# Performance work log

Measured on AMD Instinct MI355X. Metric: run time of the kernel, lower is better.

## Reference

```python
import jax, jax.numpy as jnp
import numpy as np
import math

V, D, H, L, MLP = 32000, 1024, 16, 4, 4
B, T = 2, 1024
HD = D // H
ALIBI_BIAS_MAX = 8.0
EPS = 1e-5


def _ln(x, g, b):
    m = jnp.mean(x, -1, keepdims=True)
    v = jnp.mean((x - m) ** 2, -1, keepdims=True)
    return (x - m) * jax.lax.rsqrt(v + EPS) * g + b


def setup_inputs() -> dict:
    key = jax.random.key(0)
    ks = jax.random.split(key, 12)
    s = 0.02
    inp = {
        "input_ids": jax.random.randint(ks[0], (B, T), 0, V),
        "wte": jax.random.normal(ks[1], (V, D), jnp.float32) * s,
        "ln1_g": jnp.ones((L, D), jnp.float32),
        "ln1_b": jnp.zeros((L, D), jnp.float32),
        "attn_w": jax.random.normal(ks[2], (L, 3 * D, D), jnp.float32) * s,
        "attn_b": jnp.zeros((L, 3 * D), jnp.float32),
        "proj_w": jax.random.normal(ks[3], (L, D, D), jnp.float32) * s,
        "proj_b": jnp.zeros((L, D), jnp.float32),
        "ln2_g": jnp.ones((L, D), jnp.float32),
        "ln2_b": jnp.zeros((L, D), jnp.float32),
        "fc_w": jax.random.normal(ks[4], (L, MLP * D, D), jnp.float32) * s,
        "fc_b": jnp.zeros((L, MLP * D), jnp.float32),
        "fc2_w": jax.random.normal(ks[5], (L, D, MLP * D), jnp.float32) * s,
        "fc2_b": jnp.zeros((L, D), jnp.float32),
        "lnf_g": jnp.ones((D,), jnp.float32),
        "lnf_b": jnp.zeros((D,), jnp.float32),
        "lm_head_w": jax.random.normal(ks[6], (V, D), jnp.float32) * s,
    }
    return inp


def reference(input_ids, wte, ln1_g, ln1_b, attn_w, attn_b, proj_w, proj_b,
              ln2_g, ln2_b, fc_w, fc_b, fc2_w, fc2_b, lnf_g, lnf_b, lm_head_w):
    b, t = input_ids.shape
    x = wte[input_ids]  # [B,T,D]

    # causal + ALiBi bias, [H,T,T]
    pos = jnp.arange(t)
    rel = -jnp.abs(pos[None, :] - pos[:, None]).astype(jnp.float32)  # -|i-j|
    m = jnp.arange(1, H + 1, dtype=jnp.float32) * (ALIBI_BIAS_MAX / H)
    alibi = rel[None, :, :] * (2.0 ** (-m))[:, None, None]
    causal = jnp.where(pos[None, :] > pos[:, None], -jnp.inf, 0.0)
    bias = alibi + causal[None]
    scale = 1.0 / math.sqrt(HD)

    def block(x, p):
        l1g, l1b, aw, ab, pw, pb, l2g, l2b, fw, fb, f2w, f2b = p
        h = _ln(x, l1g, l1b)
        qkv = h @ aw.T + ab  # [B,T,3D]
        q, k, v = jnp.split(qkv, 3, axis=-1)
        q = q.reshape(b, t, H, HD).transpose(0, 2, 1, 3)
        k = k.reshape(b, t, H, HD).transpose(0, 2, 1, 3)
        v = v.reshape(b, t, H, HD).transpose(0, 2, 1, 3)
        att = jnp.einsum('bhid,bhjd->bhij', q, k) * scale + bias[None]
        att = jax.nn.softmax(att, axis=-1)
        y = jnp.einsum('bhij,bhjd->bhid', att, v)
        y = y.transpose(0, 2, 1, 3).reshape(b, t, D)
        x = x + (y @ pw.T + pb)
        h2 = _ln(x, l2g, l2b)
        x = x + (jax.nn.gelu(h2 @ fw.T + fb, approximate=False) @ f2w.T + f2b)
        return x, None

    x, _ = jax.lax.scan(
        block, x,
        (ln1_g, ln1_b, attn_w, attn_b, proj_w, proj_b,
         ln2_g, ln2_b, fc_w, fc_b, fc2_w, fc2_b))
    x = _ln(x, lnf_g, lnf_b)
    logits = x @ lm_head_w.T  # [B,T,V]
    return logits
```

## Files before the change

kernel.cpp:

```cpp
#include <hip/hip_runtime.h>
#include <hip/hip_bf16.h>
#include <math.h>

typedef __hip_bfloat16 bf16;
typedef __attribute__((ext_vector_type(4))) float f32x4;
typedef __attribute__((ext_vector_type(8))) short short8;

constexpr int Bc = 2, Tc = 1024, Dc = 1024, Hc = 16, Lc = 4, MLPc = 4096, Vc = 32000, HDc = 64;

__device__ __forceinline__ unsigned short f2bu(float f) {
    __hip_bfloat16 h = __float2bfloat16(f);
    unsigned short u;
    __builtin_memcpy(&u, &h, 2);
    return u;
}

__device__ __forceinline__ void gl2lds16(const bf16* g, bf16* l) {
    __builtin_amdgcn_global_load_lds(
        (const __attribute__((address_space(1))) void*)g,
        (__attribute__((address_space(3))) void*)l, 16, 0, 0);
}

enum { EPI_BIAS_BF16 = 0, EPI_GELU = 1, EPI_RESADD = 2, EPI_F32 = 3 };

template <int EPI>
__device__ __forceinline__ void epi_store(float v, int row, int col, void* Cv,
                                          int ldc, const float* bias) {
    if constexpr (EPI == EPI_BIAS_BF16) {
        v += bias[col];
        ((bf16*)Cv)[(size_t)row * ldc + col] = __float2bfloat16(v);
    } else if constexpr (EPI == EPI_GELU) {
        v += bias[col];
        v = 0.5f * v * (1.0f + erff(v * 0.70710678118f));
        ((bf16*)Cv)[(size_t)row * ldc + col] = __float2bfloat16(v);
    } else if constexpr (EPI == EPI_RESADD) {
        float* C = (float*)Cv;
        size_t idx = (size_t)row * ldc + col;
        C[idx] += v + bias[col];
    } else if constexpr (EPI == EPI_F32) {
        ((float*)Cv)[(size_t)row * ldc + col] = v;
    }
}

template <int BM, int BN, int BK, int EPI, bool SWZG>
__global__ __launch_bounds__(256) void gemm_fast(
    const bf16* __restrict__ A, int lda,
    const bf16* __restrict__ Bm, int ldb,
    void* __restrict__ Cv, int ldc,
    const float* __restrict__ bias, int K)
{
    static_assert(BK == 64, "staging geometry assumes BK=64");
    __shared__ alignas(16) bf16 As[BM][BK];
    __shared__ alignas(16) bf16 Bs[BN][BK];

    const int tid = threadIdx.x;
    const int lane = tid & 63;
    const int w = tid >> 6;
    const int wm = w >> 1, wn = w & 1;
    constexpr int WM = BM / 2, WN = BN / 2;
    constexpr int FM = WM / 16, FN = WN / 16;
    constexpr int RPI = 512 / BK;
    constexpr int AI = BM / (4 * RPI);
    constexpr int BI = BN / (4 * RPI);

    int im, in;
    if constexpr (SWZG) {
        int nwg = gridDim.x * gridDim.y;
        int orig = blockIdx.y * gridDim.x + blockIdx.x;
        int q = nwg >> 3, rr = nwg & 7, xcd = orig & 7, lid = orig >> 3;
        int wg = (xcd < rr ? xcd * (q + 1) : rr * (q + 1) + (xcd - rr) * q) + lid;
        im = wg % gridDim.x;
        in = wg / gridDim.x;
    } else {
        im = blockIdx.y;
        in = blockIdx.x;
    }

    const bf16* Ab = A + (size_t)im * BM * lda;
    const bf16* Bb = Bm + (size_t)in * BN * ldb;

    const int sr = lane >> 3;
    const int scs = (((lane & 7) ^ sr) * 8);
    const int lr = lane & 15, lq = lane >> 4;

    f32x4 acc[FM][FN];
#pragma unroll
    for (int i = 0; i < FM; i++)
#pragma unroll
        for (int j = 0; j < FN; j++) acc[i][j] = (f32x4){0.f, 0.f, 0.f, 0.f};

    for (int k0 = 0; k0 < K; k0 += BK) {
#pragma unroll
        for (int i = 0; i < AI; i++) {
            int row = (w * AI + i) * RPI;
            gl2lds16(Ab + (size_t)(row + sr) * lda + k0 + scs, &As[row][0]);
        }
#pragma unroll
        for (int i = 0; i < BI; i++) {
            int row = (w * BI + i) * RPI;
            gl2lds16(Bb + (size_t)(row + sr) * ldb + k0 + scs, &Bs[row][0]);
        }
        __syncthreads();

#pragma unroll
        for (int kk = 0; kk < BK / 32; kk++) {
            short8 af[FM], bfr[FN];
#pragma unroll
            for (int i = 0; i < FM; i++) {
                int r = wm * WM + i * 16 + lr;
                int cb = (kk * 64 + lq * 16) ^ ((r & 7) << 4);
                af[i] = *reinterpret_cast<const short8*>((const char*)As + (size_t)r * (BK * 2) + cb);
            }
#pragma unroll
            for (int j = 0; j < FN; j++) {
                int r = wn * WN + j * 16 + lr;
                int cb = (kk * 64 + lq * 16) ^ ((r & 7) << 4);
                bfr[j] = *reinterpret_cast<const short8*>((const char*)Bs + (size_t)r * (BK * 2) + cb);
            }
#pragma unroll
            for (int i = 0; i < FM; i++)
#pragma unroll
                for (int j = 0; j < FN; j++)
                    acc[i][j] = __builtin_amdgcn_mfma_f32_16x16x32_bf16(af[i], bfr[j], acc[i][j], 0, 0, 0);
        }
        __syncthreads();
    }

#pragma unroll
    for (int i = 0; i < FM; i++)
#pragma unroll
        for (int j = 0; j < FN; j++)
#pragma unroll
            for (int r = 0; r < 4; r++) {
                int row = im * BM + wm * WM + i * 16 + lq * 4 + r;
                int col = in * BN + wn * WN + j * 16 + lr;
                epi_store<EPI>(acc[i][j][r], row, col, Cv, ldc, bias);
            }
}

__global__ __launch_bounds__(256) void flash_attn(
    const bf16* __restrict__ q, const bf16* __restrict__ kbuf,
    const bf16* __restrict__ vt, bf16* __restrict__ y)
{
    __shared__ alignas(16) bf16 Ks[128 * 64];
    __shared__ alignas(16) bf16 Vs[64 * 128];
    __shared__ alignas(16) bf16 Ps[4 * 16 * 136];

    const int tid = threadIdx.x;
    const int lane = tid & 63;
    const int w = tid >> 6;
    const int lr = lane & 15, lq = lane >> 4;
    const int qi = (int)gridDim.x - 1 - (int)blockIdx.x;
    const int z = blockIdx.y;
    const int b = z >> 4, h = z & 15;
    const float slope = exp2f(-0.5f * (float)(h + 1));

    const bf16* qz = q + (size_t)z * (Tc * HDc);
    const bf16* kz = kbuf + (size_t)z * (Tc * HDc);
    const bf16* vz = vt + (size_t)z * (HDc * Tc);

    const int rowbase = qi * 64 + w * 16;

    short8 qf[2];
#pragma unroll
    for (int kk = 0; kk < 2; kk++)
        qf[kk] = *reinterpret_cast<const short8*>(
            qz + (size_t)(rowbase + lr) * HDc + kk * 32 + lq * 8);

    float m_old[4], l_sum[4];
#pragma unroll
    for (int r = 0; r < 4; r++) { m_old[r] = -3.0e38f; l_sum[r] = 0.f; }
    f32x4 o[4];
#pragma unroll
    for (int dj = 0; dj < 4; dj++) o[dj] = (f32x4){0.f, 0.f, 0.f, 0.f};

    bf16* Pw = Ps + w * 16 * 136;

    const int nkv = (qi * 64 + 63) / 128 + 1;
    for (int kv = 0; kv < nkv; kv++) {
#pragma unroll
        for (int i = 0; i < 4; i++) {
            int rbase = w * 32 + i * 8;
            int row = rbase + (lane >> 3);
            int slot = lane & 7;
            gl2lds16(kz + (size_t)(kv * 128 + row) * HDc + ((slot ^ (row & 7)) * 8),
                     &Ks[rbase * 64]);
        }
#pragma unroll
        for (int i = 0; i < 4; i++) {
            int rbase = w * 16 + i * 4;
            int row = rbase + lq;
            gl2lds16(vz + (size_t)row * Tc + kv * 128 + ((lr ^ (row & 7)) * 8),
                     &Vs[rbase * 128]);
        }
        __syncthreads();

        f32x4 s[8];
#pragma unroll
        for (int j = 0; j < 8; j++) s[j] = (f32x4){0.f, 0.f, 0.f, 0.f};
#pragma unroll
        for (int kk = 0; kk < 2; kk++) {
#pragma unroll
            for (int j = 0; j < 8; j++) {
                int row = j * 16 + lr;
                int cb = ((kk * 4 + lq) ^ (row & 7)) << 4;
                short8 bfr = *reinterpret_cast<const short8*>(
                    (const char*)Ks + row * 128 + cb);
                s[j] = __builtin_amdgcn_mfma_f32_16x16x32_bf16(qf[kk], bfr, s[j], 0, 0, 0);
            }
        }

        float mt[4];
#pragma unroll
        for (int r = 0; r < 4; r++) mt[r] = -3.0e38f;
#pragma unroll
        for (int j = 0; j < 8; j++) {
            int col = kv * 128 + j * 16 + lr;
#pragma unroll
            for (int r = 0; r < 4; r++) {
                int rowg = rowbase + lq * 4 + r;
                float v = s[j][r] * 0.125f - (float)(rowg - col) * slope;
                v = (col > rowg) ? -3.0e38f : v;
                s[j][r] = v;
                mt[r] = fmaxf(mt[r], v);
            }
        }
#pragma unroll
        for (int r = 0; r < 4; r++)
#pragma unroll
            for (int off = 1; off < 16; off <<= 1)
                mt[r] = fmaxf(mt[r], __shfl_xor(mt[r], off));

        float f[4], rs[4];
#pragma unroll
        for (int r = 0; r < 4; r++) {
            float mn = fmaxf(m_old[r], mt[r]);
            f[r] = __expf(m_old[r] - mn);
            m_old[r] = mn;
            rs[r] = 0.f;
        }
#pragma unroll
        for (int j = 0; j < 8; j++)
#pragma unroll
            for (int r = 0; r < 4; r++) {
                float p = __expf(s[j][r] - m_old[r]);
                s[j][r] = p;
                rs[r] += p;
            }
#pragma unroll
        for (int r = 0; r < 4; r++) {
#pragma unroll
            for (int off = 1; off < 16; off <<= 1)
                rs[r] += __shfl_xor(rs[r], off);
            l_sum[r] = l_sum[r] * f[r] + rs[r];
        }

#pragma unroll
        for (int j = 0; j < 8; j++)
#pragma unroll
            for (int r = 0; r < 4; r++)
                Pw[(lq * 4 + r) * 136 + j * 16 + lr] = __float2bfloat16(s[j][r]);

#pragma unroll
        for (int dj = 0; dj < 4; dj++)
#pragma unroll
            for (int r = 0; r < 4; r++) o[dj][r] *= f[r];

        __syncthreads();

#pragma unroll
        for (int kk = 0; kk < 4; kk++) {
            short8 pa = *reinterpret_cast<const short8*>(
                (const char*)Pw + lr * 272 + kk * 64 + lq * 16);
#pragma unroll
            for (int dj = 0; dj < 4; dj++) {
                int row = dj * 16 + lr;
                int cb = ((kk * 4 + lq) ^ (row & 7)) << 4;
                short8 vb = *reinterpret_cast<const short8*>(
                    (const char*)Vs + row * 256 + cb);
                o[dj] = __builtin_amdgcn_mfma_f32_16x16x32_bf16(pa, vb, o[dj], 0, 0, 0);
            }
        }
        __syncthreads();
    }

#pragma unroll
    for (int dj = 0; dj < 4; dj++)
#pragma unroll
        for (int r = 0; r < 4; r++) {
            int rowg = rowbase + lq * 4 + r;
            float outv = o[dj][r] / l_sum[r];
            y[((size_t)b * Tc + rowg) * Dc + h * HDc + dj * 16 + lr] =
                __float2bfloat16(outv);
        }
}

__global__ __launch_bounds__(256) void f2b8(const float* __restrict__ in,
                                            bf16* __restrict__ out, long n) {
    long i = ((long)blockIdx.x * 256 + threadIdx.x) * 8;
    if (i >= n) return;
    float4 a = *reinterpret_cast<const float4*>(in + i);
    float4 b = *reinterpret_cast<const float4*>(in + i + 4);
    unsigned long long p0 = (unsigned long long)f2bu(a.x) |
                            ((unsigned long long)f2bu(a.y) << 16) |
                            ((unsigned long long)f2bu(a.z) << 32) |
                            ((unsigned long long)f2bu(a.w) << 48);
    unsigned long long p1 = (unsigned long long)f2bu(b.x) |
                            ((unsigned long long)f2bu(b.y) << 16) |
                            ((unsigned long long)f2bu(b.z) << 32) |
                            ((unsigned long long)f2bu(b.w) << 48);
    *reinterpret_cast<unsigned long long*>(out + i) = p0;
    *reinterpret_cast<unsigned long long*>(out + i + 4) = p1;
}

__global__ __launch_bounds__(256) void embed_kernel(const int* __restrict__ ids,
                                                    const float* __restrict__ wte,
                                                    float* __restrict__ x) {
    int row = blockIdx.x;
    int t = threadIdx.x;
    int id = ids[row];
    reinterpret_cast<float4*>(x + (size_t)row * Dc)[t] =
        reinterpret_cast<const float4*>(wte + (size_t)id * Dc)[t];
}

__global__ __launch_bounds__(256) void ln_kernel(const float* __restrict__ x,
                                                 const float* __restrict__ g,
                                                 const float* __restrict__ b,
                                                 bf16* __restrict__ out) {
    int row = blockIdx.x;
    int t = threadIdx.x;
    const float4 v = reinterpret_cast<const float4*>(x + (size_t)row * Dc)[t];
    float s = v.x + v.y + v.z + v.w;
    float s2 = v.x * v.x + v.y * v.y + v.z * v.z + v.w * v.w;
#pragma unroll
    for (int o = 32; o > 0; o >>= 1) {
        s += __shfl_down(s, o);
        s2 += __shfl_down(s2, o);
    }
    __shared__ float sm[8];
    int wid = t >> 6, ln = t & 63;
    if (ln == 0) { sm[wid] = s; sm[4 + wid] = s2; }
    __syncthreads();
    if (t == 0) {
        float ts = sm[0] + sm[1] + sm[2] + sm[3];
        float ts2 = sm[4] + sm[5] + sm[6] + sm[7];
        sm[0] = ts; sm[4] = ts2;
    }
    __syncthreads();
    float mean = sm[0] * (1.0f / Dc);
    float var = sm[4] * (1.0f / Dc) - mean * mean;
    float rstd = rsqrtf(var + 1e-5f);
    int c0 = t * 4;
    float vv[4] = {v.x, v.y, v.z, v.w};
    unsigned long long p = 0;
#pragma unroll
    for (int j = 0; j < 4; j++) {
        float val = (vv[j] - mean) * rstd * g[c0 + j] + b[c0 + j];
        p |= (unsigned long long)f2bu(val) << (16 * j);
    }
    *reinterpret_cast<unsigned long long*>(out + (size_t)row * Dc + c0) = p;
}

__global__ __launch_bounds__(256) void unpack_qk(const bf16* __restrict__ qkv,
                                                 bf16* __restrict__ q,
                                                 bf16* __restrict__ k) {
    int idx = blockIdx.x * 256 + threadIdx.x;
    int bt = idx / 128;
    int c = idx % 128;
    int b = bt / Tc, t = bt % Tc;
    int h = c >> 3;
    int hd = (c & 7) * 8;
    size_t dst = (((size_t)(b * Hc + h) * Tc + t) * HDc + hd) / 8;
    const int4* src = reinterpret_cast<const int4*>(qkv + (size_t)bt * 3 * Dc);
    reinterpret_cast<int4*>(q)[dst] = src[c];
    reinterpret_cast<int4*>(k)[dst] = src[128 + c];
}

__global__ __launch_bounds__(256) void unpack_vt(const bf16* __restrict__ qkv,
                                                 bf16* __restrict__ vt) {
    int idx = blockIdx.x * 256 + threadIdx.x;
    int t = idx & (Tc - 1);
    int rest = idx >> 10;
    int hd = rest & 63;
    int zh = rest >> 6;
    int b = zh >> 4, h = zh & 15;
    vt[idx] = qkv[((size_t)(b * Tc + t)) * 3 * Dc + 2 * Dc + h * HDc + hd];
}

extern "C" void kernel_launch(void* const* d_in, const int* in_sizes, int n_in,
                              void* d_out, int out_size, void* d_ws, size_t ws_size,
                              hipStream_t stream) {
    const int* ids = (const int*)d_in[0];
    const float* wte = (const float*)d_in[1];
    const float* ln1g = (const float*)d_in[2];
    const float* ln1b = (const float*)d_in[3];
    const float* attw = (const float*)d_in[4];
    const float* attb = (const float*)d_in[5];
    const float* projw = (const float*)d_in[6];
    const float* projb = (const float*)d_in[7];
    const float* ln2g = (const float*)d_in[8];
    const float* ln2b = (const float*)d_in[9];
    const float* fcw = (const float*)d_in[10];
    const float* fcb = (const float*)d_in[11];
    const float* fc2w = (const float*)d_in[12];
    const float* fc2b = (const float*)d_in[13];
    const float* lnfg = (const float*)d_in[14];
    const float* lnfb = (const float*)d_in[15];
    const float* lmw = (const float*)d_in[16];

    const int M = Bc * Tc;
    char* ws = (char*)d_ws;
    size_t off = 0;
    auto carve = [&](size_t bytes) { char* p = ws + off; off += (bytes + 255) & ~(size_t)255; return p; };

    float* x = (float*)carve((size_t)M * Dc * 4);
    bf16* h = (bf16*)carve((size_t)M * Dc * 2);
    bf16* qkv = (bf16*)carve((size_t)M * 3 * Dc * 2);
    bf16* q = (bf16*)carve((size_t)Bc * Hc * Tc * HDc * 2);
    bf16* kb = (bf16*)carve((size_t)Bc * Hc * Tc * HDc * 2);
    bf16* vt = (bf16*)carve((size_t)Bc * Hc * Tc * HDc * 2);
    bf16* y = (bf16*)carve((size_t)M * Dc * 2);
    bf16* mlp = (bf16*)carve((size_t)M * MLPc * 2);
    size_t base_end = off;

    const long nWL = (long)3 * Dc * Dc + (long)Dc * Dc + (long)MLPc * Dc + (long)Dc * MLPc;
    const long nLM = (long)Vc * Dc;
    bool has_wl = ws_size >= base_end + (size_t)nWL * 2;
    bf16* wl = nullptr;
    if (has_wl) wl = (bf16*)carve((size_t)nWL * 2);
    bool has_wlm = has_wl && ws_size >= off + (size_t)nLM * 2;
    bf16* wlm = nullptr;
    if (has_wlm) wlm = (bf16*)carve((size_t)nLM * 2);

    bf16* aw_b = wl;
    bf16* pw_b = wl ? wl + (size_t)3 * Dc * Dc : nullptr;
    bf16* fw_b = pw_b ? pw_b + (size_t)Dc * Dc : nullptr;
    bf16* f2w_b = fw_b ? fw_b + (size_t)MLPc * Dc : nullptr;

    embed_kernel<<<M, 256, 0, stream>>>(ids, wte, x);

    if (has_wlm)
        f2b8<<<(int)(nLM / 8 / 256), 256, 0, stream>>>(lmw, wlm, nLM);
    if (!has_wl) {
    }

    for (int l = 0; l < Lc; l++) {
        if (has_wl) {
            f2b8<<<(int)((long)3 * Dc * Dc / 8 / 256), 256, 0, stream>>>(
                attw + (size_t)l * 3 * Dc * Dc, aw_b, (long)3 * Dc * Dc);
            f2b8<<<(int)((long)Dc * Dc / 8 / 256), 256, 0, stream>>>(
                projw + (size_t)l * Dc * Dc, pw_b, (long)Dc * Dc);
            f2b8<<<(int)((long)MLPc * Dc / 8 / 256), 256, 0, stream>>>(
                fcw + (size_t)l * MLPc * Dc, fw_b, (long)MLPc * Dc);
            f2b8<<<(int)((long)Dc * MLPc / 8 / 256), 256, 0, stream>>>(
                fc2w + (size_t)l * Dc * MLPc, f2w_b, (long)Dc * MLPc);
        }

        ln_kernel<<<M, 256, 0, stream>>>(x, ln1g + l * Dc, ln1b + l * Dc, h);

        gemm_fast<128, 128, 64, EPI_BIAS_BF16, true>
            <<<dim3(M / 128, 3 * Dc / 128, 1), 256, 0, stream>>>(
                h, Dc, aw_b, Dc, qkv, 3 * Dc, attb + l * 3 * Dc, Dc);

        unpack_qk<<<(M * Dc / 8) / 256, 256, 0, stream>>>(qkv, q, kb);
        unpack_vt<<<(Bc * Hc * HDc * Tc) / 256, 256, 0, stream>>>(qkv, vt);

        flash_attn<<<dim3(Tc / 64, Bc * Hc), 256, 0, stream>>>(q, kb, vt, y);

        gemm_fast<128, 128, 64, EPI_RESADD, true>
            <<<dim3(M / 128, Dc / 128, 1), 256, 0, stream>>>(
                y, Dc, pw_b, Dc, x, Dc, projb + l * Dc, Dc);

        ln_kernel<<<M, 256, 0, stream>>>(x, ln2g + l * Dc, ln2b + l * Dc, h);

        gemm_fast<128, 128, 64, EPI_GELU, true>
            <<<dim3(M / 128, MLPc / 128, 1), 256, 0, stream>>>(
                h, Dc, fw_b, Dc, mlp, MLPc, fcb + l * MLPc, Dc);

        gemm_fast<128, 128, 64, EPI_RESADD, true>
            <<<dim3(M / 128, Dc / 128, 1), 256, 0, stream>>>(
                mlp, MLPc, f2w_b, MLPc, x, Dc, fc2b + l * Dc, MLPc);
    }

    ln_kernel<<<M, 256, 0, stream>>>(x, lnfg, lnfb, h);

    gemm_fast<128, 128, 64, EPI_F32, true>
        <<<dim3(M / 128, Vc / 128, 1), 256, 0, stream>>>(
            h, Dc, wlm, Dc, (float*)d_out, Vc, nullptr, Dc);
}
```

Measured before the change: 1.298 ms.

## Double-buffer GEMM LDS, fuse QKV unpack, batch weight conversion into output buffer

The GEMM main loop now double-buffers the LDS tiles and issues the next tile's global-to-LDS loads before computing on the current one, so load latency can overlap MFMA work. The q/k unpack and the V transpose are merged into one kernel, and the V transpose gathers eight elements per thread and writes them with vector stores. All per-layer weight fp32-to-bf16 conversions are hoisted into four large launches that write into the output buffer as scratch before the final GEMM overwrites it. A fallback GEMM that converts fp32 weights inside the kernel is added for the case where the workspace is too small. There is only one barrier per k-tile, so the prefetch into the other buffer may race with waves still reading that buffer from the previous iteration.

New measurement: 1.309 ms. No clear change (+0.8%).

```diff
diff --git a/kernel.cpp b/kernel.cpp
--- a/kernel.cpp
+++ b/kernel.cpp
@@ -50,8 +50,8 @@
     const float* __restrict__ bias, int K)
 {
     static_assert(BK == 64, "staging geometry assumes BK=64");
-    __shared__ alignas(16) bf16 As[BM][BK];
-    __shared__ alignas(16) bf16 Bs[BN][BK];
+    __shared__ alignas(16) bf16 As[2][BM][BK];
+    __shared__ alignas(16) bf16 Bs[2][BN][BK];
 
     const int tid = threadIdx.x;
     const int lane = tid & 63;
@@ -89,19 +89,29 @@
 #pragma unroll
         for (int j = 0; j < FN; j++) acc[i][j] = (f32x4){0.f, 0.f, 0.f, 0.f};
 
-    for (int k0 = 0; k0 < K; k0 += BK) {
+    auto stage = [&](int buf, int k0) {
 #pragma unroll
         for (int i = 0; i < AI; i++) {
             int row = (w * AI + i) * RPI;
-            gl2lds16(Ab + (size_t)(row + sr) * lda + k0 + scs, &As[row][0]);
+            gl2lds16(Ab + (size_t)(row + sr) * lda + k0 + scs, &As[buf][row][0]);
         }
 #pragma unroll
         for (int i = 0; i < BI; i++) {
             int row = (w * BI + i) * RPI;
-            gl2lds16(Bb + (size_t)(row + sr) * ldb + k0 + scs, &Bs[row][0]);
-        }
-        __syncthreads();
-
+            gl2lds16(Bb + (size_t)(row + sr) * ldb + k0 + scs, &Bs[buf][row][0]);
+        }
+    };
+
+    const int NT = K / BK;
+    stage(0, 0);
+    __syncthreads();
+
+    for (int t = 0; t < NT; t++) {
+        const int cur = t & 1;
+        if (t + 1 < NT) stage(cur ^ 1, (t + 1) * BK);
+
+        const char* Abase = (const char*)&As[cur][0][0];
+        const char* Bbase = (const char*)&Bs[cur][0][0];
 #pragma unroll
         for (int kk = 0; kk < BK / 32; kk++) {
             short8 af[FM], bfr[FN];
@@ -109,13 +119,13 @@
             for (int i = 0; i < FM; i++) {
                 int r = wm * WM + i * 16 + lr;
                 int cb = (kk * 64 + lq * 16) ^ ((r & 7) << 4);
-                af[i] = *reinterpret_cast<const short8*>((const char*)As + (size_t)r * (BK * 2) + cb);
+                af[i] = *reinterpret_cast<const short8*>(Abase + (size_t)r * (BK * 2) + cb);
             }
 #pragma unroll
             for (int j = 0; j < FN; j++) {
                 int r = wn * WN + j * 16 + lr;
                 int cb = (kk * 64 + lq * 16) ^ ((r & 7) << 4);
-                bfr[j] = *reinterpret_cast<const short8*>((const char*)Bs + (size_t)r * (BK * 2) + cb);
+                bfr[j] = *reinterpret_cast<const short8*>(Bbase + (size_t)r * (BK * 2) + cb);
             }
 #pragma unroll
             for (int i = 0; i < FM; i++)
@@ -134,6 +144,84 @@
             for (int r = 0; r < 4; r++) {
                 int row = im * BM + wm * WM + i * 16 + lq * 4 + r;
                 int col = in * BN + wn * WN + j * 16 + lr;
+                epi_store<EPI>(acc[i][j][r], row, col, Cv, ldc, bias);
+            }
+}
+
+template <int BM, int BN, int BK, int EPI>
+__global__ __launch_bounds__(256) void gemm_bt_f32(
+    const bf16* __restrict__ A, int lda,
+    const float* __restrict__ Bm, int ldb,
+    void* __restrict__ Cv, int ldc,
+    const float* __restrict__ bias, int K)
+{
+    constexpr int BKP = BK + 8;
+    __shared__ bf16 As[BM][BKP];
+    __shared__ bf16 Bs[BN][BKP];
+    const int tid = threadIdx.x;
+    const int lane = tid & 63;
+    const int w = tid >> 6;
+    const int wm = w >> 1, wn = w & 1;
+    constexpr int WM = BM / 2, WN = BN / 2;
+    constexpr int FM = WM / 16, FN = WN / 16;
+    const int bx = blockIdx.x, by = blockIdx.y;
+    const bf16* Ab = A + (size_t)by * BM * lda;
+    const float* Bb = Bm + (size_t)bx * BN * ldb;
+    f32x4 acc[FM][FN];
+#pragma unroll
+    for (int i = 0; i < FM; i++)
+#pragma unroll
+        for (int j = 0; j < FN; j++) acc[i][j] = (f32x4){0.f, 0.f, 0.f, 0.f};
+    const int lr = lane & 15, lq = lane >> 4;
+    for (int k0 = 0; k0 < K; k0 += BK) {
+        constexpr int AC = (BM * BK) / (256 * 8);
+#pragma unroll
+        for (int i = 0; i < AC; i++) {
+            int c = tid + i * 256;
+            int row = c / (BK / 8);
+            int kc = (c % (BK / 8)) * 8;
+            *reinterpret_cast<int4*>(&As[row][kc]) =
+                *reinterpret_cast<const int4*>(Ab + (size_t)row * lda + k0 + kc);
+        }
+        constexpr int BC = (BN * BK) / (256 * 4);
+#pragma unroll
+        for (int i = 0; i < BC; i++) {
+            int c = tid + i * 256;
+            int row = c / (BK / 4);
+            int kc = (c % (BK / 4)) * 4;
+            float4 v = *reinterpret_cast<const float4*>(Bb + (size_t)row * ldb + k0 + kc);
+            unsigned long long p = (unsigned long long)f2bu(v.x) |
+                                   ((unsigned long long)f2bu(v.y) << 16) |
+                                   ((unsigned long long)f2bu(v.z) << 32) |
+                                   ((unsigned long long)f2bu(v.w) << 48);
+            *reinterpret_cast<unsigned long long*>(&Bs[row][kc]) = p;
+        }
+        __syncthreads();
+#pragma unroll
+        for (int kk = 0; kk < BK / 32; kk++) {
+            short8 af[FM], bfr[FN];
+#pragma unroll
+            for (int i = 0; i < FM; i++)
+                af[i] = *reinterpret_cast<const short8*>(&As[wm * WM + i * 16 + lr][kk * 32 + lq * 8]);
+#pragma unroll
+            for (int j = 0; j < FN; j++)
+                bfr[j] = *reinterpret_cast<const short8*>(&Bs[wn * WN + j * 16 + lr][kk * 32 + lq * 8]);
+#pragma unroll
+            for (int i = 0; i < FM; i++)
+#pragma unroll
+                for (int j = 0; j < FN; j++)
+                    acc[i][j] = __builtin_amdgcn_mfma_f32_16x16x32_bf16(af[i], bfr[j], acc[i][j], 0, 0, 0);
+        }
+        __syncthreads();
+    }
+#pragma unroll
+    for (int i = 0; i < FM; i++)
+#pragma unroll
+        for (int j = 0; j < FN; j++)
+#pragma unroll
+            for (int r = 0; r < 4; r++) {
+                int row = by * BM + wm * WM + i * 16 + lq * 4 + r;
+                int col = bx * BN + wn * WN + j * 16 + lr;
                 epi_store<EPI>(acc[i][j][r], row, col, Cv, ldc, bias);
             }
 }
@@ -361,30 +449,46 @@
     *reinterpret_cast<unsigned long long*>(out + (size_t)row * Dc + c0) = p;
 }
 
-__global__ __launch_bounds__(256) void unpack_qk(const bf16* __restrict__ qkv,
-                                                 bf16* __restrict__ q,
-                                                 bf16* __restrict__ k) {
+__global__ __launch_bounds__(256) void unpack_qkv(const bf16* __restrict__ qkv,
+                                                  bf16* __restrict__ q,
+                                                  bf16* __restrict__ k,
+                                                  bf16* __restrict__ vt) {
     int idx = blockIdx.x * 256 + threadIdx.x;
-    int bt = idx / 128;
-    int c = idx % 128;
-    int b = bt / Tc, t = bt % Tc;
-    int h = c >> 3;
-    int hd = (c & 7) * 8;
-    size_t dst = (((size_t)(b * Hc + h) * Tc + t) * HDc + hd) / 8;
-    const int4* src = reinterpret_cast<const int4*>(qkv + (size_t)bt * 3 * Dc);
-    reinterpret_cast<int4*>(q)[dst] = src[c];
-    reinterpret_cast<int4*>(k)[dst] = src[128 + c];
-}
-
-__global__ __launch_bounds__(256) void unpack_vt(const bf16* __restrict__ qkv,
-                                                 bf16* __restrict__ vt) {
-    int idx = blockIdx.x * 256 + threadIdx.x;
-    int t = idx & (Tc - 1);
-    int rest = idx >> 10;
-    int hd = rest & 63;
-    int zh = rest >> 6;
-    int b = zh >> 4, h = zh & 15;
-    vt[idx] = qkv[((size_t)(b * Tc + t)) * 3 * Dc + 2 * Dc + h * HDc + hd];
+    {
+        int bt = idx >> 7;
+        int c = idx & 127;
+        int b = bt >> 10, t = bt & (Tc - 1);
+        int h = c >> 3;
+        int hd = (c & 7) * 8;
+        size_t dst = (((size_t)(b * Hc + h) * Tc + t) * HDc + hd) / 8;
+        const int4* src = reinterpret_cast<const int4*>(qkv + (size_t)bt * 3 * Dc);
+        reinterpret_cast<int4*>(q)[dst] = src[c];
+        reinterpret_cast<int4*>(k)[dst] = src[128 + c];
+    }
+    {
+        int t0 = (idx & 127) * 8;
+        int rest = idx >> 7;
+        int hd = rest & 63;
+        int z = rest >> 6;
+        int b = z >> 4, h = z & 15;
+        const bf16* src = qkv + ((size_t)b * Tc) * 3 * Dc + 2 * Dc + h * HDc + hd;
+        unsigned long long p0 = 0, p1 = 0;
+#pragma unroll
+        for (int i = 0; i < 4; i++) {
+            unsigned short u;
+            __builtin_memcpy(&u, src + (size_t)(t0 + i) * 3 * Dc, 2);
+            p0 |= (unsigned long long)u << (16 * i);
+        }
+#pragma unroll
+        for (int i = 0; i < 4; i++) {
+            unsigned short u;
+            __builtin_memcpy(&u, src + (size_t)(t0 + 4 + i) * 3 * Dc, 2);
+            p1 |= (unsigned long long)u << (16 * i);
+        }
+        bf16* dst = vt + ((size_t)z * HDc + hd) * Tc + t0;
+        *reinterpret_cast<unsigned long long*>(dst) = p0;
+        *reinterpret_cast<unsigned long long*>(dst + 4) = p1;
+    }
 }
 
 extern "C" void kernel_launch(void* const* d_in, const int* in_sizes, int n_in,
@@ -421,40 +525,35 @@
     bf16* vt = (bf16*)carve((size_t)Bc * Hc * Tc * HDc * 2);
     bf16* y = (bf16*)carve((size_t)M * Dc * 2);
     bf16* mlp = (bf16*)carve((size_t)M * MLPc * 2);
-    size_t base_end = off;
-
-    const long nWL = (long)3 * Dc * Dc + (long)Dc * Dc + (long)MLPc * Dc + (long)Dc * MLPc;
+
     const long nLM = (long)Vc * Dc;
-    bool has_wl = ws_size >= base_end + (size_t)nWL * 2;
-    bf16* wl = nullptr;
-    if (has_wl) wl = (bf16*)carve((size_t)nWL * 2);
-    bool has_wlm = has_wl && ws_size >= off + (size_t)nLM * 2;
+    bool has_wlm = ws_size >= off + (size_t)nLM * 2;
     bf16* wlm = nullptr;
     if (has_wlm) wlm = (bf16*)carve((size_t)nLM * 2);
 
-    bf16* aw_b = wl;
-    bf16* pw_b = wl ? wl + (size_t)3 * Dc * Dc : nullptr;
-    bf16* fw_b = pw_b ? pw_b + (size_t)Dc * Dc : nullptr;
-    bf16* f2w_b = fw_b ? fw_b + (size_t)MLPc * Dc : nullptr;
+    const long nAW = (long)Lc * 3 * Dc * Dc;
+    const long nPW = (long)Lc * Dc * Dc;
+    const long nFW = (long)Lc * MLPc * Dc;
+    const long nF2W = (long)Lc * Dc * MLPc;
+    bf16* awAll = (bf16*)d_out;
+    bf16* pwAll = awAll + nAW;
+    bf16* fwAll = pwAll + nPW;
+    bf16* f2wAll = fwAll + nFW;
 
     embed_kernel<<<M, 256, 0, stream>>>(ids, wte, x);
 
+    f2b8<<<(int)(nAW / 8 / 256), 256, 0, stream>>>(attw, awAll, nAW);
+    f2b8<<<(int)(nPW / 8 / 256), 256, 0, stream>>>(projw, pwAll, nPW);
+    f2b8<<<(int)(nFW / 8 / 256), 256, 0, stream>>>(fcw, fwAll, nFW);
+    f2b8<<<(int)(nF2W / 8 / 256), 256, 0, stream>>>(fc2w, f2wAll, nF2W);
     if (has_wlm)
         f2b8<<<(int)(nLM / 8 / 256), 256, 0, stream>>>(lmw, wlm, nLM);
-    if (!has_wl) {
-    }
 
     for (int l = 0; l < Lc; l++) {
-        if (has_wl) {
-            f2b8<<<(int)((long)3 * Dc * Dc / 8 / 256), 256, 0, stream>>>(
-                attw + (size_t)l * 3 * Dc * Dc, aw_b, (long)3 * Dc * Dc);
-            f2b8<<<(int)((long)Dc * Dc / 8 / 256), 256, 0, stream>>>(
-                projw + (size_t)l * Dc * Dc, pw_b, (long)Dc * Dc);
-            f2b8<<<(int)((long)MLPc * Dc / 8 / 256), 256, 0, stream>>>(
-                fcw + (size_t)l * MLPc * Dc, fw_b, (long)MLPc * Dc);
-            f2b8<<<(int)((long)Dc * MLPc / 8 / 256), 256, 0, stream>>>(
-                fc2w + (size_t)l * Dc * MLPc, f2w_b, (long)Dc * MLPc);
-        }
+        bf16* aw_b = awAll + (size_t)l * 3 * Dc * Dc;
+        bf16* pw_b = pwAll + (size_t)l * Dc * Dc;
+        bf16* fw_b = fwAll + (size_t)l * MLPc * Dc;
+        bf16* f2w_b = f2wAll + (size_t)l * Dc * MLPc;
 
         ln_kernel<<<M, 256, 0, stream>>>(x, ln1g + l * Dc, ln1b + l * Dc, h);
 
@@ -462,8 +561,7 @@
             <<<dim3(M / 128, 3 * Dc / 128, 1), 256, 0, stream>>>(
                 h, Dc, aw_b, Dc, qkv, 3 * Dc, attb + l * 3 * Dc, Dc);
 
-        unpack_qk<<<(M * Dc / 8) / 256, 256, 0, stream>>>(qkv, q, kb);
-        unpack_vt<<<(Bc * Hc * HDc * Tc) / 256, 256, 0, stream>>>(qkv, vt);
+        unpack_qkv<<<(M * Dc / 8) / 256, 256, 0, stream>>>(qkv, q, kb, vt);
 
         flash_attn<<<dim3(Tc / 64, Bc * Hc), 256, 0, stream>>>(q, kb, vt, y);
 
@@ -484,7 +582,12 @@
 
     ln_kernel<<<M, 256, 0, stream>>>(x, lnfg, lnfb, h);
 
-    gemm_fast<128, 128, 64, EPI_F32, true>
-        <<<dim3(M / 128, Vc / 128, 1), 256, 0, stream>>>(
-            h, Dc, wlm, Dc, (float*)d_out, Vc, nullptr, Dc);
-}
+    if (has_wlm)
+        gemm_fast<128, 128, 64, EPI_F32, true>
+            <<<dim3(M / 128, Vc / 128, 1), 256, 0, stream>>>(
+                h, Dc, wlm, Dc, (float*)d_out, Vc, nullptr, Dc);
+    else
+        gemm_bt_f32<128, 128, 64, EPI_F32>
+            <<<dim3(Vc / 128, M / 128, 1), 256, 0, stream>>>(
+                h, Dc, lmw, Dc, (float*)d_out, Vc, nullptr, Dc);
+}
```
